# Performance work log

Measured on AMD Instinct MI355X. Metric: run time of the kernel, lower is better.

## Reference

```python
import jax, jax.numpy as jnp
import numpy as np

D_MODEL = 1024
N_HEADS = 16
B, T = 2, 2048


def setup_inputs() -> dict:
    key = jax.random.key(0)
    ks = jax.random.split(key, 5)
    scale = 1.0 / np.sqrt(D_MODEL)
    return {
        "x": jax.random.normal(ks[0], (B, T, D_MODEL), dtype=jnp.float32),
        "W_q": jax.random.normal(ks[1], (D_MODEL, D_MODEL), dtype=jnp.float32) * scale,
        "W_k": jax.random.normal(ks[2], (D_MODEL, D_MODEL), dtype=jnp.float32) * scale,
        "W_v": jax.random.normal(ks[3], (D_MODEL, D_MODEL), dtype=jnp.float32) * scale,
        "W_o": jax.random.normal(ks[4], (D_MODEL, D_MODEL), dtype=jnp.float32) * scale,
    }


def reference(x, W_q, W_k, W_v, W_o):
    Bn, Tn, D = x.shape
    H = N_HEADS
    Dh = D // H
    # nn.Linear(x) = x @ W.T ; weights stored as [out, in]
    q = (x @ W_q.T).reshape(Bn, Tn, H, Dh).transpose(0, 2, 1, 3)  # [B,H,T,Dh]
    k = (x @ W_k.T).reshape(Bn, Tn, H, Dh).transpose(0, 2, 1, 3)
    v = (x @ W_v.T).reshape(Bn, Tn, H, Dh).transpose(0, 2, 1, 3)
    scores = jnp.einsum("bhqd,bhkd->bhqk", q, k) / np.sqrt(Dh).astype(np.float32)
    attn = jax.nn.softmax(scores, axis=-1)  # [B,H,T,T]
    out = jnp.einsum("bhqk,bhkd->bhqd", attn, v)  # [B,H,T,Dh]
    out = out.transpose(0, 2, 1, 3).reshape(Bn, Tn, D)
    return out @ W_o.T
```

## Files before the change

### kernel.cpp

```cpp
#include <hip/hip_runtime.h>
#include <stdint.h>
#include <stddef.h>


typedef __bf16  bf16x8  __attribute__((ext_vector_type(8)));
typedef __bf16  bf16x4  __attribute__((ext_vector_type(4)));
typedef float   floatx4 __attribute__((ext_vector_type(4)));
typedef short   short4v __attribute__((ext_vector_type(4)));

#define DEV static __device__ __forceinline__

DEV void ld_g2l16(const void* g, void* l) {
    __builtin_amdgcn_global_load_lds(
        (__attribute__((address_space(1))) void*)g,
        (__attribute__((address_space(3))) void*)l,
        16, 0, 0);
}

DEV floatx4 mfma16(bf16x4 a, bf16x4 b, floatx4 c) {
#if defined(__HIP_DEVICE_COMPILE__)
    return __builtin_amdgcn_mfma_f32_16x16x16bf16_1k(
        __builtin_bit_cast(short4v, a), __builtin_bit_cast(short4v, b),
        c, 0, 0, 0);
#else
    (void)a; (void)b;
    return c;
#endif
}

#define WK_SCALE 0.18033688011112042f

__global__ __launch_bounds__(256) void cvt_all(
    const float* __restrict__ x,
    const float* __restrict__ wq, const float* __restrict__ wk,
    const float* __restrict__ wv, const float* __restrict__ wo,
    __bf16* __restrict__ xb,
    __bf16* __restrict__ wqb, __bf16* __restrict__ wkb,
    __bf16* __restrict__ wvb, __bf16* __restrict__ wob)
{
    unsigned u = blockIdx.x * 256u + threadIdx.x;
    const float* src;
    __bf16* dst;
    unsigned off;
    float mul = 1.0f;
    if (u < 1048576u) {
        src = x; dst = xb; off = u;
    } else {
        unsigned u2 = u - 1048576u;
        unsigned sel = u2 >> 18;
        off = u2 & 0x3FFFFu;
        src = (sel == 0) ? wq : (sel == 1) ? wk : (sel == 2) ? wv : wo;
        dst = (sel == 0) ? wqb : (sel == 1) ? wkb : (sel == 2) ? wvb : wob;
        if (sel == 1) mul = WK_SCALE;
    }
    float4 f = *(const float4*)(src + (size_t)off * 4);
    bf16x4 o = { (__bf16)(f.x * mul), (__bf16)(f.y * mul),
                 (__bf16)(f.z * mul), (__bf16)(f.w * mul) };
    *(bf16x4*)(dst + (size_t)off * 4) = o;
}

template<int BM, int NMAT, bool OUT_F32, bool TR_V>
__global__ __launch_bounds__(256) void gemm_bt(
    const __bf16* __restrict__ A,
    const __bf16* __restrict__ B0, const __bf16* __restrict__ B1,
    const __bf16* __restrict__ B2,
    void* __restrict__ C0, void* __restrict__ C1, void* __restrict__ C2)
{
    constexpr int Kd = 1024;
    constexpr int N  = 1024;
    constexpr int MI = BM / 32;
    constexpr int NA = BM / 64;
    __shared__ __bf16 As[BM * 32];
    __shared__ __bf16 Bs[128 * 32];

    const int t    = threadIdx.x;
    const int wid  = __builtin_amdgcn_readfirstlane(t >> 6);
    const int lane = t & 63;
    const int quad = lane >> 4;
    const int l15  = lane & 15;

    const int bx  = blockIdx.x;
    const int mat = (NMAT > 1) ? (bx >> 3) : 0;
    const int bn  = (NMAT > 1) ? (bx & 7)  : bx;
    const int bm  = blockIdx.y;
    const __bf16* Bm = (mat == 0) ? B0 : (mat == 1) ? B1 : B2;

    const __bf16* pA[NA];
    const __bf16* pB[2];
#pragma unroll
    for (int i = 0; i < NA; ++i) {
        int c    = i * 256 + t;
        int row  = c >> 2;
        int g    = (c & 3) ^ ((row >> 1) & 3);
        pA[i] = A + (size_t)(bm * BM + row) * Kd + g * 8;
    }
#pragma unroll
    for (int i = 0; i < 2; ++i) {
        int c    = i * 256 + t;
        int row  = c >> 2;
        int g    = (c & 3) ^ ((row >> 1) & 3);
        pB[i] = Bm + (size_t)(bn * 128 + row) * Kd + g * 8;
    }

    const int wm = wid >> 1;
    const int wn = wid & 1;
    const int slotr = quad ^ ((l15 >> 1) & 3);

    floatx4 acc[MI][4];
    const floatx4 z = { 0.f, 0.f, 0.f, 0.f };
#pragma unroll
    for (int i = 0; i < MI; ++i)
#pragma unroll
        for (int j = 0; j < 4; ++j) acc[i][j] = z;

    for (int kb = 0; kb < Kd; kb += 32) {
        __syncthreads();
#pragma unroll
        for (int i = 0; i < NA; ++i)
            ld_g2l16(pA[i] + kb, (char*)As + i * 4096 + wid * 1024);
#pragma unroll
        for (int i = 0; i < 2; ++i)
            ld_g2l16(pB[i] + kb, (char*)Bs + i * 4096 + wid * 1024);
        __syncthreads();

        bf16x8 af[MI], bf[4];
#pragma unroll
        for (int i = 0; i < MI; ++i) {
            int rowA = wm * (BM / 2) + i * 16 + l15;
            af[i] = *(const bf16x8*)&As[rowA * 32 + slotr * 8];
        }
#pragma unroll
        for (int j = 0; j < 4; ++j) {
            int rowB = wn * 64 + j * 16 + l15;
            bf[j] = *(const bf16x8*)&Bs[rowB * 32 + slotr * 8];
        }
#pragma unroll
        for (int i = 0; i < MI; ++i)
#pragma unroll
            for (int j = 0; j < 4; ++j)
                acc[i][j] = __builtin_amdgcn_mfma_f32_16x16x32_bf16(
                    af[i], bf[j], acc[i][j], 0, 0, 0);
    }

    const int row0 = bm * BM + wm * (BM / 2);
    const int col0 = bn * 128 + wn * 64;

    if (TR_V && mat == 2) {
        __bf16* Vt = (__bf16*)C2;
        const int bq    = bm >> 4;
        const int tloc0 = (row0 & 2047) + quad * 4;
#pragma unroll
        for (int i = 0; i < MI; ++i)
#pragma unroll
            for (int j = 0; j < 4; ++j) {
                int col = col0 + j * 16 + l15;
                int hh  = col >> 6, dh = col & 63;
                bf16x4 v = { (__bf16)acc[i][j][0], (__bf16)acc[i][j][1],
                             (__bf16)acc[i][j][2], (__bf16)acc[i][j][3] };
                *(bf16x4*)(Vt + ((size_t)(bq * 16 + hh) * 64 + dh) * 2048
                              + tloc0 + i * 16) = v;
            }
    } else {
        void* Cv = (mat == 0) ? C0 : (mat == 1) ? C1 : C2;
#pragma unroll
        for (int i = 0; i < MI; ++i)
#pragma unroll
            for (int j = 0; j < 4; ++j)
#pragma unroll
                for (int r = 0; r < 4; ++r) {
                    int grow = row0 + i * 16 + quad * 4 + r;
                    int gcol = col0 + j * 16 + l15;
                    if (OUT_F32)
                        ((float*)Cv)[(size_t)grow * N + gcol] = acc[i][j][r];
                    else
                        ((__bf16*)Cv)[(size_t)grow * N + gcol] =
                            (__bf16)acc[i][j][r];
                }
    }
}

__global__ __launch_bounds__(256, 2) void flash_kernel(
    const __bf16* __restrict__ Q, const __bf16* __restrict__ K,
    const __bf16* __restrict__ Vt, __bf16* __restrict__ O)
{
    __shared__ __bf16 Qs[128 * 64];
    __shared__ __bf16 Ks[2][64 * 64];
    __shared__ __bf16 Vs[2][64 * 64];

    const int t    = threadIdx.x;
    const int wid  = __builtin_amdgcn_readfirstlane(t >> 6);
    const int half = wid >> 1;
    const int wsub = wid & 1;
    const int lane = t & 63;
    const int quad = lane >> 4;
    const int l15  = lane & 15;
    const int flat = blockIdx.y * 16 + blockIdx.x;
    const int swz  = (flat & 7) * 64 + (flat >> 3);
    const int qt   = swz & 15;
    const int bh   = swz >> 4;
    const int b    = bh >> 4, h = bh & 15;

#pragma unroll
    for (int i = 0; i < 4; ++i) {
        int c = i * 256 + t;
        int row = c >> 3;
        int g   = (c & 7) ^ (row & 7);
        ld_g2l16(Q + (size_t)(b * 2048 + qt * 128 + row) * 1024 + h * 64 + g * 8,
                 (char*)Qs + i * 4096 + wid * 1024);
    }

    const __bf16* pK[2];
    const __bf16* pV[2];
#pragma unroll
    for (int i = 0; i < 2; ++i) {
        int c = i * 256 + t;
        int srow = c >> 3;
        int sg   = (c & 7) ^ (srow & 7);
        pK[i] = K  + (size_t)(b * 2048 + srow) * 1024 + h * 64 + sg * 8;
        pV[i] = Vt + (size_t)(bh * 64 + srow) * 2048 + sg * 8;
    }

    __syncthreads();

    bf16x8 qf[4][2];
#pragma unroll
    for (int nb = 0; nb < 4; ++nb)
#pragma unroll
        for (int ks = 0; ks < 2; ++ks) {
            int row  = wsub * 64 + nb * 16 + l15;
            int slot = (ks * 4 + quad) ^ (row & 7);
            qf[nb][ks] = *(const bf16x8*)&Qs[row * 64 + slot * 8];
        }

    int koff[2];
#pragma unroll
    for (int ks = 0; ks < 2; ++ks)
        koff[ks] = l15 * 128 + (((ks * 4 + quad) ^ (l15 & 7)) << 4);
    int voff[4];
#pragma unroll
    for (int k16 = 0; k16 < 4; ++k16)
        voff[k16] = l15 * 128 + (((k16 * 2 + (quad >> 1)) ^ (l15 & 7)) << 4)
                  + (quad & 1) * 8;

    const floatx4 z = { 0.f, 0.f, 0.f, 0.f };
    floatx4 o[4][4];
#pragma unroll
    for (int nb = 0; nb < 4; ++nb)
#pragma unroll
        for (int nd = 0; nd < 4; ++nd) o[nb][nd] = z;
    float lsum[4] = { 0.f, 0.f, 0.f, 0.f };

    for (int it = 0; it < 16; ++it) {
        __syncthreads();
#pragma unroll
        for (int i = 0; i < 2; ++i) {
            ld_g2l16(pK[i] + (size_t)it * 65536,
                     (char*)Ks[0] + i * 4096 + wid * 1024);
            ld_g2l16(pK[i] + (size_t)(16 + it) * 65536,
                     (char*)Ks[1] + i * 4096 + wid * 1024);
            ld_g2l16(pV[i] + it * 64,
                     (char*)Vs[0] + i * 4096 + wid * 1024);
            ld_g2l16(pV[i] + (16 + it) * 64,
                     (char*)Vs[1] + i * 4096 + wid * 1024);
        }
        __syncthreads();

        const char* kbase = (const char*)Ks[half];
        const char* vbase = (const char*)Vs[half];
#pragma unroll
        for (int kt16 = 0; kt16 < 4; ++kt16) {
            floatx4 s[4] = { z, z, z, z };
#pragma unroll
            for (int ks = 0; ks < 2; ++ks) {
                bf16x8 kf = *(const bf16x8*)(kbase + kt16 * 2048 + koff[ks]);
#pragma unroll
                for (int nb = 0; nb < 4; ++nb)
                    s[nb] = __builtin_amdgcn_mfma_f32_16x16x32_bf16(
                        kf, qf[nb][ks], s[nb], 0, 0, 0);
            }
            bf16x4 pb[4];
#pragma unroll
            for (int nb = 0; nb < 4; ++nb) {
                float p0 = __builtin_amdgcn_exp2f(s[nb][0]);
                float p1 = __builtin_amdgcn_exp2f(s[nb][1]);
                float p2 = __builtin_amdgcn_exp2f(s[nb][2]);
                float p3 = __builtin_amdgcn_exp2f(s[nb][3]);
                lsum[nb] += (p0 + p1) + (p2 + p3);
                bf16x4 pw = { (__bf16)p0, (__bf16)p1, (__bf16)p2, (__bf16)p3 };
                pb[nb] = pw;
            }
#pragma unroll
            for (int nd = 0; nd < 4; ++nd) {
                bf16x4 va = *(const bf16x4*)(vbase + nd * 2048 + voff[kt16]);
#pragma unroll
                for (int nb = 0; nb < 4; ++nb)
                    o[nb][nd] = mfma16(va, pb[nb], o[nb][nd]);
            }
        }
    }

    __syncthreads();
    float* obuf = (wsub == 0) ? (float*)&Ks[0][0] : (float*)&Vs[0][0];
    float* lbuf = (float*)&Qs[0] + wsub * 256;
    if (half == 1) {
#pragma unroll
        for (int nb = 0; nb < 4; ++nb)
#pragma unroll
            for (int nd = 0; nd < 4; ++nd)
                *(floatx4*)(obuf + (nb * 4 + nd) * 256 + lane * 4) = o[nb][nd];
#pragma unroll
        for (int nb = 0; nb < 4; ++nb) lbuf[nb * 64 + lane] = lsum[nb];
    }
    __syncthreads();
    if (half == 0) {
#pragma unroll
        for (int nb = 0; nb < 4; ++nb)
#pragma unroll
            for (int nd = 0; nd < 4; ++nd)
                o[nb][nd] += *(const floatx4*)(obuf + (nb * 4 + nd) * 256
                                               + lane * 4);
#pragma unroll
        for (int nb = 0; nb < 4; ++nb) {
            lsum[nb] += lbuf[nb * 64 + lane];
            lsum[nb] += __shfl_xor(lsum[nb], 16);
            lsum[nb] += __shfl_xor(lsum[nb], 32);
        }
#pragma unroll
        for (int nb = 0; nb < 4; ++nb) {
            float inv = 1.f / lsum[nb];
            int token = qt * 128 + wsub * 64 + nb * 16 + l15;
#pragma unroll
            for (int nd = 0; nd < 4; ++nd) {
                bf16x4 ov = { (__bf16)(o[nb][nd][0] * inv),
                              (__bf16)(o[nb][nd][1] * inv),
                              (__bf16)(o[nb][nd][2] * inv),
                              (__bf16)(o[nb][nd][3] * inv) };
                *(bf16x4*)(O + (size_t)(b * 2048 + token) * 1024
                             + h * 64 + nd * 16 + quad * 4) = ov;
            }
        }
    }
}

extern "C" void kernel_launch(void* const* d_in, const int* in_sizes, int n_in,
                              void* d_out, int out_size, void* d_ws, size_t ws_size,
                              hipStream_t stream)
{
    const float* x  = (const float*)d_in[0];
    const float* wq = (const float*)d_in[1];
    const float* wk = (const float*)d_in[2];
    const float* wv = (const float*)d_in[3];
    const float* wo = (const float*)d_in[4];

    char* ws = (char*)d_ws;
    __bf16* xb  = (__bf16*)(ws + 0);
    __bf16* wqb = (__bf16*)(ws + 8388608);
    __bf16* wkb = (__bf16*)(ws + 10485760);
    __bf16* wvb = (__bf16*)(ws + 12582912);
    __bf16* wob = (__bf16*)(ws + 14680064);
    __bf16* Qb  = (__bf16*)(ws + 16777216);
    __bf16* Kb  = (__bf16*)(ws + 25165824);
    __bf16* Vtb = (__bf16*)(ws + 33554432);
    __bf16* Ob  = xb;

    cvt_all<<<8192, 256, 0, stream>>>(x, wq, wk, wv, wo, xb, wqb, wkb, wvb, wob);

    gemm_bt<128, 3, false, true><<<dim3(24, 32), 256, 0, stream>>>(
        xb, wqb, wkb, wvb, (void*)Qb, (void*)Kb, (void*)Vtb);

    flash_kernel<<<dim3(16, 32), 256, 0, stream>>>(Qb, Kb, Vtb, Ob);

    gemm_bt<64, 1, true, false><<<dim3(8, 64), 256, 0, stream>>>(
        Ob, wob, nullptr, nullptr, d_out, nullptr, nullptr);
}
```

Baseline: 176.7 us.

## Double K-step per barrier in GEMMs and swizzle blocks across XCDs

The projection GEMMs now load two 32-wide K slices into separate LDS buffers per iteration. This halves the number of barrier pairs across the K loop. Block indices are also remapped so that consecutive logical tiles land on the same XCD, which is meant to improve L2 reuse of A and B panels. The cost is twice the LDS per block, which may reduce occupancy. There is still no real overlap of loads with compute.

```diff
diff --git a/kernel.cpp b/kernel.cpp
--- a/kernel.cpp
+++ b/kernel.cpp
@@ -59,7 +59,7 @@
     *(bf16x4*)(dst + (size_t)off * 4) = o;
 }
 
-template<int BM, int NMAT, bool OUT_F32, bool TR_V>
+template<int BM, int NMAT, bool OUT_F32, bool TR_V, int NBX, int NBY>
 __global__ __launch_bounds__(256) void gemm_bt(
     const __bf16* __restrict__ A,
     const __bf16* __restrict__ B0, const __bf16* __restrict__ B1,
@@ -70,8 +70,8 @@
     constexpr int N  = 1024;
     constexpr int MI = BM / 32;
     constexpr int NA = BM / 64;
-    __shared__ __bf16 As[BM * 32];
-    __shared__ __bf16 Bs[128 * 32];
+    __shared__ __bf16 As[2][BM * 32];
+    __shared__ __bf16 Bs[2][128 * 32];
 
     const int t    = threadIdx.x;
     const int wid  = __builtin_amdgcn_readfirstlane(t >> 6);
@@ -79,10 +79,15 @@
     const int quad = lane >> 4;
     const int l15  = lane & 15;
 
-    const int bx  = blockIdx.x;
-    const int mat = (NMAT > 1) ? (bx >> 3) : 0;
-    const int bn  = (NMAT > 1) ? (bx & 7)  : bx;
-    const int bm  = blockIdx.y;
+    constexpr int TOT   = NBX * NBY;
+    constexpr int CHUNK = TOT / 8;
+    static_assert(TOT % 8 == 0, "grid must split evenly over 8 XCDs");
+    const int flat = blockIdx.y * NBX + blockIdx.x;
+    const int swz  = (flat & 7) * CHUNK + (flat >> 3);
+    const int vbx  = swz % NBX;
+    const int mat  = (NMAT > 1) ? (vbx >> 3) : 0;
+    const int bn   = (NMAT > 1) ? (vbx & 7)  : vbx;
+    const int bm   = swz / NBX;
     const __bf16* Bm = (mat == 0) ? B0 : (mat == 1) ? B1 : B2;
 
     const __bf16* pA[NA];
@@ -113,33 +118,41 @@
 #pragma unroll
         for (int j = 0; j < 4; ++j) acc[i][j] = z;
 
-    for (int kb = 0; kb < Kd; kb += 32) {
+    for (int kb = 0; kb < Kd; kb += 64) {
         __syncthreads();
 #pragma unroll
-        for (int i = 0; i < NA; ++i)
-            ld_g2l16(pA[i] + kb, (char*)As + i * 4096 + wid * 1024);
-#pragma unroll
-        for (int i = 0; i < 2; ++i)
-            ld_g2l16(pB[i] + kb, (char*)Bs + i * 4096 + wid * 1024);
+        for (int h = 0; h < 2; ++h) {
+#pragma unroll
+            for (int i = 0; i < NA; ++i)
+                ld_g2l16(pA[i] + kb + h * 32,
+                         (char*)&As[h][0] + i * 4096 + wid * 1024);
+#pragma unroll
+            for (int i = 0; i < 2; ++i)
+                ld_g2l16(pB[i] + kb + h * 32,
+                         (char*)&Bs[h][0] + i * 4096 + wid * 1024);
+        }
         __syncthreads();
 
-        bf16x8 af[MI], bf[4];
-#pragma unroll
-        for (int i = 0; i < MI; ++i) {
-            int rowA = wm * (BM / 2) + i * 16 + l15;
-            af[i] = *(const bf16x8*)&As[rowA * 32 + slotr * 8];
-        }
-#pragma unroll
-        for (int j = 0; j < 4; ++j) {
-            int rowB = wn * 64 + j * 16 + l15;
-            bf[j] = *(const bf16x8*)&Bs[rowB * 32 + slotr * 8];
-        }
-#pragma unroll
-        for (int i = 0; i < MI; ++i)
-#pragma unroll
-            for (int j = 0; j < 4; ++j)
-                acc[i][j] = __builtin_amdgcn_mfma_f32_16x16x32_bf16(
-                    af[i], bf[j], acc[i][j], 0, 0, 0);
+#pragma unroll
+        for (int h = 0; h < 2; ++h) {
+            bf16x8 af[MI], bf[4];
+#pragma unroll
+            for (int i = 0; i < MI; ++i) {
+                int rowA = wm * (BM / 2) + i * 16 + l15;
+                af[i] = *(const bf16x8*)&As[h][rowA * 32 + slotr * 8];
+            }
+#pragma unroll
+            for (int j = 0; j < 4; ++j) {
+                int rowB = wn * 64 + j * 16 + l15;
+                bf[j] = *(const bf16x8*)&Bs[h][rowB * 32 + slotr * 8];
+            }
+#pragma unroll
+            for (int i = 0; i < MI; ++i)
+#pragma unroll
+                for (int j = 0; j < 4; ++j)
+                    acc[i][j] = __builtin_amdgcn_mfma_f32_16x16x32_bf16(
+                        af[i], bf[j], acc[i][j], 0, 0, 0);
+        }
     }
 
     const int row0 = bm * BM + wm * (BM / 2);
@@ -365,11 +378,11 @@
 
     cvt_all<<<8192, 256, 0, stream>>>(x, wq, wk, wv, wo, xb, wqb, wkb, wvb, wob);
 
-    gemm_bt<128, 3, false, true><<<dim3(24, 32), 256, 0, stream>>>(
+    gemm_bt<128, 3, false, true, 24, 32><<<dim3(24, 32), 256, 0, stream>>>(
         xb, wqb, wkb, wvb, (void*)Qb, (void*)Kb, (void*)Vtb);
 
     flash_kernel<<<dim3(16, 32), 256, 0, stream>>>(Qb, Kb, Vtb, Ob);
 
-    gemm_bt<64, 1, true, false><<<dim3(8, 64), 256, 0, stream>>>(
+    gemm_bt<64, 1, true, false, 8, 64><<<dim3(8, 64), 256, 0, stream>>>(
         Ob, wob, nullptr, nullptr, d_out, nullptr, nullptr);
 }
```

New measurement: 182.5 us. +3.3%, slower.
